# Optimization experiments

Hardware: AMD Instinct MI355X
Metric: run time of the kernel (lower is better)

The kernel has to match this reference:

```python
import jax, jax.numpy as jnp
import numpy as np

H = 2        # num_heads
C = 128      # in_channels
K_ORDER = 4
BETA = 0.5


def _gcn_conv(x, row, col, deg_inv, n):
    # x: [N, H, C]; adj_t = D^{-1} A^T where A[row, col] = 1
    # (adj_t @ x)[c] = deg_inv[c] * sum_{e: col_e == c} x[row_e]
    msg = x[row]  # [E, H, C]
    agg = jax.ops.segment_sum(msg, col, num_segments=n)  # [N, H, C]
    return agg * deg_inv[:, None, None]


def _attn_conv(qs, ks, vs):
    # linear (kernelized) attention, non-block path
    n = qs.shape[0]
    kvs = jnp.einsum('lhm,lhd->hmd', ks, vs)            # [H, C, C]
    qkvs = jnp.einsum('nhm,hmd->nhd', qs, kvs)          # [N, H, C]
    vs_sum = vs.sum(axis=0)                             # [H, C]
    num = qkvs + vs_sum[None, :, :]
    ks_sum = ks.sum(axis=0)                             # [H, C]
    qks_sum = jnp.einsum('nhm,hm->nh', qs, ks_sum)[:, :, None]  # [N, H, 1]
    den = qks_sum + jnp.asarray(n, qs.dtype)
    return num / den


def setup_inputs() -> dict:
    key = jax.random.key(0)
    ks = jax.random.split(key, 8)
    N, E = 100000, 1600000
    x = jax.random.normal(ks[0], (N, C), jnp.float32)
    edge_index = jax.random.randint(ks[1], (2, E), 0, N, jnp.int64)
    s_in = 1.0 / np.sqrt(C)
    s_out = 1.0 / np.sqrt(H * C * (K_ORDER + 1))
    Wq_w = jax.random.normal(ks[2], (C, H * C), jnp.float32) * s_in
    Wq_b = jax.random.normal(ks[3], (H * C,), jnp.float32) * s_in
    Wk_w = jax.random.normal(ks[4], (C, H * C), jnp.float32) * s_in
    Wk_b = jax.random.normal(ks[5], (H * C,), jnp.float32) * s_in
    Wo_w = jax.random.normal(ks[6], (H * C * (K_ORDER + 1), C), jnp.float32) * s_out
    Wo_b = jax.random.normal(ks[7], (C,), jnp.float32) * s_out
    return {"x": x, "edge_index": edge_index, "Wq_w": Wq_w, "Wq_b": Wq_b,
            "Wk_w": Wk_w, "Wk_b": Wk_b, "Wo_w": Wo_w, "Wo_b": Wo_b}


def reference(x, edge_index, Wq_w, Wq_b, Wk_w, Wk_b, Wo_w, Wo_b):
    n = x.shape[0]
    row, col = edge_index[0], edge_index[1]
    # normalized adjacency D^{-1} A^T (pow(-1.0) in the source, not -0.5)
    deg = jax.ops.segment_sum(jnp.ones(row.shape[0], x.dtype), col, num_segments=n)
    deg_inv = jnp.where(deg > 0, 1.0 / deg, 0.0)

    query = (x @ Wq_w + Wq_b).reshape(n, H, C)
    key = (x @ Wk_w + Wk_b).reshape(n, H, C)
    qs = query / jnp.linalg.norm(query, axis=2, keepdims=True)
    ks = key / jnp.linalg.norm(key, axis=2, keepdims=True)

    x0 = jnp.broadcast_to(x[:, None, :], (n, H, C))  # [N, H, C]
    terms = [x0]
    for _ in range(K_ORDER):
        prev = terms[-1]
        gcn_i = _gcn_conv(prev, row, col, deg_inv, n)
        attn_i = _attn_conv(qs, ks, prev)
        terms.append(BETA * gcn_i + attn_i)
    xcat = jnp.concatenate(terms, axis=-1)  # [N, H, C*(K+1)]
    xcat = xcat.reshape(n, H * C * (K_ORDER + 1))
    return (xcat @ Wo_w + Wo_b) / H
```

## Files before the change

### kernel.cpp

```cpp
#include <hip/hip_runtime.h>

#define THREADS 256
#define NB 512
#define SEGCAP 6144
#define CSB 512

typedef __attribute__((ext_vector_type(8))) short short8;
typedef __attribute__((ext_vector_type(4))) float f32x4;

__device__ __forceinline__ float bf2f(unsigned short u) {
    union { unsigned int i; float f; } v;
    v.i = ((unsigned int)u) << 16;
    return v.f;
}
__device__ __forceinline__ unsigned short f2bf(float f) {
    union { float f; unsigned int i; } v;
    v.f = f;
    unsigned int r = (v.i + 0x7FFFu + ((v.i >> 16) & 1u)) >> 16;
    return (unsigned short)r;
}
__device__ __forceinline__ float4 ld4f(const float* p) {
    return *reinterpret_cast<const float4*>(p);
}
__device__ __forceinline__ float4 ld4f(const unsigned short* p) {
// ... 47 lines not shown
    for (int off = 1; off < NB; off <<= 1) {
        int add = (t >= off) ? s[t - off] : 0;
        __syncthreads();
        s[t] += add;
        __syncthreads();
    }
    gbase[t] = s[t] - v;
    gcursor[t] = s[t] - v;
}

__global__ __launch_bounds__(256) void k_part(const int* __restrict__ eb, int E,
                                              const int* __restrict__ mode, int N, int CW, int epb,
                                              int* __restrict__ gcursor, uint2* __restrict__ ebuf) {
    __shared__ int hist[NB];
    __shared__ int base[NB];
    for (int i = threadIdx.x; i < NB; i += 256) hist[i] = 0;
    __syncthreads();
    int m = *mode;
    int e0 = blockIdx.x * epb;
    int e1 = min(e0 + epb, E);
    for (int e = e0 + threadIdx.x; e < e1; e += 256) {
        int c = edge_get(eb, E, m, 1, e);
        if ((unsigned)c < (unsigned)N) atomicAdd(&hist[c / CW], 1);
    }
    __syncthreads();
    for (int i = threadIdx.x; i < NB; i += 256) {
        int h = hist[i];
        base[i] = h ? atomicAdd(&gcursor[i], h) : 0;
        hist[i] = 0;
    }
    __syncthreads();
    for (int e = e0 + threadIdx.x; e < e1; e += 256) {
        int c = edge_get(eb, E, m, 1, e);
        if ((unsigned)c < (unsigned)N) {
            int r = edge_get(eb, E, m, 0, e);
            if ((unsigned)r >= (unsigned)N) r = 0;
            int b = c / CW;
            int li = atomicAdd(&hist[b], 1);
            ebuf[(size_t)base[b] + li] = make_uint2((unsigned)r, (unsigned)c);
        }
    }
}

__global__ __launch_bounds__(256) void k_build(const uint2* __restrict__ ebuf,
                                               const int* __restrict__ gbase,
                                               const int* __restrict__ gcnt, int N, int CW,
                                               int* __restrict__ cnt, int* __restrict__ offs,
                                               float* __restrict__ deg_inv, int* __restrict__ csr) {
    __shared__ int hist[256];
    __shared__ int pfx[256];
    __shared__ int seg[SEGCAP];
    const int b = blockIdx.x;
    const int col0 = b * CW;
    const int ncols = min(CW, N - col0);
    if (ncols <= 0) return;
    const int ebase = gbase[b], ecnt = gcnt[b];
    const int t = threadIdx.x;
    for (int i = t; i < 256; i += 256) hist[i] = 0;
    __syncthreads();
    for (int e = t; e < ecnt; e += 256) {
        uint2 rc = ebuf[(size_t)ebase + e];
        atomicAdd(&hist[rc.y - col0], 1);
    }
    __syncthreads();
    int v = (t < ncols) ? hist[t] : 0;
    pfx[t] = v;
    __syncthreads();
    for (int off = 1; off < 256; off <<= 1) {
        int add = (t >= off) ? pfx[t - off] : 0;
        __syncthreads();
        pfx[t] += add;
        __syncthreads();
    }
    int excl = pfx[t] - v;
    if (t < ncols) {
        cnt[col0 + t] = v;
        offs[col0 + t] = ebase + excl;
        deg_inv[col0 + t] = (v > 0) ? 1.0f / (float)v : 0.0f;
    }
    __syncthreads();
    if (t < 256) hist[t] = (t < ncols) ? excl : 0;
    __syncthreads();
    if (ecnt <= SEGCAP) {
        for (int e = t; e < ecnt; e += 256) {
            uint2 rc = ebuf[(size_t)ebase + e];
            int li = atomicAdd(&hist[rc.y - col0], 1);
            seg[li] = (int)rc.x;
        }
        __syncthreads();
        for (int e = t; e < ecnt; e += 256) csr[(size_t)ebase + e] = seg[e];
    } else {
        for (int e = t; e < ecnt; e += 256) {
            uint2 rc = ebuf[(size_t)ebase + e];
            int li = atomicAdd(&hist[rc.y - col0], 1);
            csr[(size_t)ebase + li] = (int)rc.x;
        }
    }
}

__global__ __launch_bounds__(256) void k_prep_wqk(const float* __restrict__ Wq,
                                                  const float* __restrict__ Wk,
                                                  unsigned short* __restrict__ WqkT) {
    int i = blockIdx.x * 256 + threadIdx.x;
    if (i < 512 * 128) {
        int oc = i >> 7, k = i & 127;
        float v = (oc < 256) ? Wq[k * 256 + oc] : Wk[k * 256 + (oc - 256)];
        WqkT[i] = f2bf(v);
    }
}

__global__ __launch_bounds__(256) void k_prep_wo(const float* __restrict__ Wo,
                                                 unsigned short* __restrict__ WoT) {
    int i = blockIdx.x * 256 + threadIdx.x;
    if (i < 1280 * 128) {
        int r = i >> 7, j = i & 127;
        WoT[(size_t)j * 1280 + r] = f2bf(Wo[i]);
    }
}

__global__ __launch_bounds__(256) void k_prep_wo0(const float* __restrict__ Wo,
                                                  unsigned short* __restrict__ WoT0) {
    int i = blockIdx.x * 256 + threadIdx.x;
    if (i < 16384) {
        int j = i >> 7, c = i & 127;
        WoT0[i] = f2bf(Wo[(size_t)c * 128 + j] + Wo[(size_t)(640 + c) * 128 + j]);
    }
}

__global__ __launch_bounds__(256) void k_proj(const float* __restrict__ x,
                                              const unsigned short* __restrict__ WqkT,
                                              const float* __restrict__ bq,
                                              const float* __restrict__ bk,
                                              unsigned short* __restrict__ qs,
                                              unsigned short* __restrict__ ks, int N) {
    __shared__ unsigned short xs[64 * 128];
    __shared__ unsigned short os[64 * 256];
    const int t = threadIdx.x;
    const int n0 = blockIdx.x * 64;
#pragma unroll
    for (int i = 0; i < 4; i++) {
        int chunk = i * 256 + t;
        int r = chunk >> 4, c0 = (chunk & 15) * 8;
        float4 a0 = make_float4(0.f, 0.f, 0.f, 0.f), a1 = a0;
        if (n0 + r < N) {
            a0 = ld4f(&x[(size_t)(n0 + r) * 128 + c0]);
            a1 = ld4f(&x[(size_t)(n0 + r) * 128 + c0 + 4]);
        }
        short8 v = {(short)f2bf(a0.x), (short)f2bf(a0.y), (short)f2bf(a0.z), (short)f2bf(a0.w),
                    (short)f2bf(a1.x), (short)f2bf(a1.y), (short)f2bf(a1.z), (short)f2bf(a1.w)};
        int byte = r * 256 + ((c0 * 2) ^ ((r & 7) << 4));
        *reinterpret_cast<short8*>(reinterpret_cast<char*>(xs) + byte) = v;
    }
    __syncthreads();
    const int w = t >> 6, l = t & 63, lrow = l & 15, lhi = l >> 4;
    f32x4 acc[4][8];
    const f32x4 fz = {0.f, 0.f, 0.f, 0.f};
#pragma unroll
    for (int mt = 0; mt < 4; mt++)
#pragma unroll
        for (int nt = 0; nt < 8; nt++) acc[mt][nt] = fz;

    for (int kk = 0; kk < 4; kk++) {
        int kb = kk * 32 + lhi * 8;
        short8 af[4];
#pragma unroll
        for (int mt = 0; mt < 4; mt++) {
            int r = mt * 16 + lrow;
            af[mt] = *reinterpret_cast<const short8*>(
                reinterpret_cast<const char*>(xs) + r * 256 + ((kb * 2) ^ ((r & 7) << 4)));
        }
#pragma unroll
        for (int nt = 0; nt < 8; nt++) {
            int oc = w * 128 + nt * 16 + lrow;
            short8 bf = *reinterpret_cast<const short8*>(&WqkT[(size_t)oc * 128 + kb]);
#pragma unroll
            for (int mt = 0; mt < 4; mt++)
                acc[mt][nt] = __builtin_amdgcn_mfma_f32_16x16x32_bf16(af[mt], bf, acc[mt][nt], 0, 0, 0);
        }
    }
#pragma unroll
    for (int nt = 0; nt < 8; nt++) {
        int oc = w * 128 + nt * 16 + lrow;
        float b = (oc < 256) ? bq[oc] : bk[oc - 256];
#pragma unroll
        for (int mt = 0; mt < 4; mt++)
#pragma unroll
            for (int reg = 0; reg < 4; reg++) acc[mt][nt][reg] += b;
    }
    const int hc = (w & 1) * 128;
    float rv[4][4];
#pragma unroll
    for (int mt = 0; mt < 4; mt++) {
        float ss[4] = {0.f, 0.f, 0.f, 0.f};
#pragma unroll
        for (int nt = 0; nt < 8; nt++)
#pragma unroll
            for (int reg = 0; reg < 4; reg++) ss[reg] += acc[mt][nt][reg] * acc[mt][nt][reg];
#pragma unroll
        for (int m_ = 1; m_ < 16; m_ <<= 1)
#pragma unroll
            for (int reg = 0; reg < 4; reg++) ss[reg] += __shfl_xor(ss[reg], m_);
#pragma unroll
        for (int reg = 0; reg < 4; reg++) rv[mt][reg] = rsqrtf(ss[reg]);
    }
    for (int pass = 0; pass < 2; pass++) {
        if ((w >> 1) == pass) {
#pragma unroll
            for (int mt = 0; mt < 4; mt++)
#pragma unroll
                for (int reg = 0; reg < 4; reg++) {
                    int r = mt * 16 + lhi * 4 + reg;
#pragma unroll
                    for (int nt = 0; nt < 8; nt++)
                        os[r * 256 + hc + nt * 16 + lrow] = f2bf(acc[mt][nt][reg] * rv[mt][reg]);
                }
        }
        __syncthreads();
        unsigned short* dstg = pass ? ks : qs;
#pragma unroll
        for (int i = 0; i < 8; i++) {
            int chunk = i * 256 + t;
            int r = chunk >> 5, c = (chunk & 31) * 8;
            int n = n0 + r;
            if (n < N)
                *reinterpret_cast<short8*>(&dstg[(size_t)n * 256 + c]) =
                    *reinterpret_cast<const short8*>(&os[r * 256 + c]);
        }
        __syncthreads();
    }
}

__global__ __launch_bounds__(256) void k_colsum(const unsigned short* __restrict__ ks, int N,
                                                float* __restrict__ part) {
    __shared__ float red[8][256];
    const int t = threadIdx.x;
    const int rl = t >> 5;
    const int c0 = (t & 31) * 8;
    const int stride = (N + CSB - 1) / CSB;
    const int r0 = blockIdx.x * stride;
    const int rend = min(r0 + stride, N);
    float s[8] = {0.f, 0.f, 0.f, 0.f, 0.f, 0.f, 0.f, 0.f};
    int r = r0 + rl;
    for (; r + 24 < rend; r += 32) {
        short8 v0 = *reinterpret_cast<const short8*>(&ks[(size_t)(r + 0) * 256 + c0]);
        short8 v1 = *reinterpret_cast<const short8*>(&ks[(size_t)(r + 8) * 256 + c0]);
        short8 v2 = *reinterpret_cast<const short8*>(&ks[(size_t)(r + 16) * 256 + c0]);
        short8 v3 = *reinterpret_cast<const short8*>(&ks[(size_t)(r + 24) * 256 + c0]);
#pragma unroll
        for (int j = 0; j < 8; j++)
            s[j] += bf2f((unsigned short)v0[j]) + bf2f((unsigned short)v1[j]) +
                    bf2f((unsigned short)v2[j]) + bf2f((unsigned short)v3[j]);
    }
    for (; r < rend; r += 8) {
        short8 v = *reinterpret_cast<const short8*>(&ks[(size_t)r * 256 + c0]);
#pragma unroll
        for (int j = 0; j < 8; j++) s[j] += bf2f((unsigned short)v[j]);
    }
#pragma unroll
    for (int j = 0; j < 8; j++) red[rl][c0 + j] = s[j];
    __syncthreads();
    float tot = 0.f;
#pragma unroll
    for (int g = 0; g < 8; g++) tot += red[g][t];
    part[blockIdx.x * 256 + t] = tot;
}

__global__ __launch_bounds__(256) void k_colsum2(const float* __restrict__ part,
                                                 float* __restrict__ ks_sum) {
    const int t = threadIdx.x;
    float s0 = 0.f, s1 = 0.f, s2 = 0.f, s3 = 0.f;
    for (int b = 0; b < CSB; b += 4) {
        s0 += part[(b + 0) * 256 + t];
        s1 += part[(b + 1) * 256 + t];
        s2 += part[(b + 2) * 256 + t];
        s3 += part[(b + 3) * 256 + t];
    }
    ks_sum[t] = (s0 + s1) + (s2 + s3);
}

__global__ __launch_bounds__(256) void k_den(const unsigned short* __restrict__ qs,
                                             const float* __restrict__ ks_sum,
                                             float* __restrict__ den, int N) {
    int w = threadIdx.x >> 6, lane = threadIdx.x & 63;
    int n = blockIdx.x * 4 + w;
    if (n >= N) return;
    float4 q = ld4f(&qs[(size_t)n * 256 + lane * 4]);
    float4 kv = *reinterpret_cast<const float4*>(&ks_sum[lane * 4]);
    float s = q.x * kv.x + q.y * kv.y + q.z * kv.z + q.w * kv.w;
#pragma unroll
    for (int off = 1; off < 32; off <<= 1) s += __shfl_xor(s, off);
    if ((lane & 31) == 0) den[n * 2 + (lane >> 5)] = s + (float)N;
}

__device__ __forceinline__ short8 frag_ld(const unsigned short* tile, int kb, int col) {
    const char* b = reinterpret_cast<const char*>(tile);
    int cb = (col * 2) ^ (((kb >> 3) & 3) << 5);
    short8 r;
#pragma unroll
    for (int i = 0; i < 8; i++)
        r[i] = (short)*reinterpret_cast<const unsigned short*>(b + (kb + i) * 512 + cb);
    return r;
}

template <typename TV>
__global__ __launch_bounds__(256) void k_kvs2(const unsigned short* __restrict__ ks,
                                              const TV* __restrict__ vs, int vstride, int vmask,
                                              float* __restrict__ partial,
                                              float* __restrict__ pvsum, int rows_per, int N) {
    __shared__ unsigned short kt[32 * 256];
    __shared__ unsigned short vt[32 * 256];
    __shared__ float vred[8][256];
    const int t = threadIdx.x;
    const int w = t >> 6, l = t & 63, lrow = l & 15, lhi = l >> 4;
    const int h = w >> 1, mhalf = w & 1;
    const int r0 = blockIdx.x * rows_per;
    const int rend = min(r0 + rows_per, N);

    const f32x4 fz = {0.f, 0.f, 0.f, 0.f};
    f32x4 acc[4][8];
#pragma unroll
    for (int mt = 0; mt < 4; mt++)
#pragma unroll
        for (int nt = 0; nt < 8; nt++) acc[mt][nt] = fz;
    float vsum8[8] = {0.f, 0.f, 0.f, 0.f, 0.f, 0.f, 0.f, 0.f};

    for (int c0 = r0; c0 < rend; c0 += 32) {
#pragma unroll
        for (int i = 0; i < 4; i++) {
            int chunk = i * 256 + t;
            int n = chunk >> 5, cc = (chunk & 31) * 8;
            short8 v = {0, 0, 0, 0, 0, 0, 0, 0};
            if (c0 + n < rend)
                v = *reinterpret_cast<const short8*>(&ks[(size_t)(c0 + n) * 256 + cc]);
            *reinterpret_cast<short8*>(reinterpret_cast<char*>(kt) + n * 512 +
                                       ((cc * 2) ^ (((n >> 3) & 3) << 5))) = v;
        }
#pragma unroll
        for (int i = 0; i < 4; i++) {
            int chunk = i * 256 + t;
            int n = chunk >> 5, cc = (chunk & 31) * 8;
            float4 a0 = make_float4(0.f, 0.f, 0.f, 0.f), a1 = a0;
            if (c0 + n < rend) {
                a0 = ld4f(&vs[(size_t)(c0 + n) * vstride + (cc & vmask)]);
                a1 = ld4f(&vs[(size_t)(c0 + n) * vstride + ((cc + 4) & vmask)]);
            }
            unsigned short u0 = f2bf(a0.x), u1 = f2bf(a0.y), u2 = f2bf(a0.z), u3 = f2bf(a0.w);
            unsigned short u4 = f2bf(a1.x), u5 = f2bf(a1.y), u6 = f2bf(a1.z), u7 = f2bf(a1.w);
            vsum8[0] += bf2f(u0); vsum8[1] += bf2f(u1); vsum8[2] += bf2f(u2); vsum8[3] += bf2f(u3);
            vsum8[4] += bf2f(u4); vsum8[5] += bf2f(u5); vsum8[6] += bf2f(u6); vsum8[7] += bf2f(u7);
            short8 v = {(short)u0, (short)u1, (short)u2, (short)u3,
                        (short)u4, (short)u5, (short)u6, (short)u7};
            *reinterpret_cast<short8*>(reinterpret_cast<char*>(vt) + n * 512 +
                                       ((cc * 2) ^ (((n >> 3) & 3) << 5))) = v;
        }
        __syncthreads();
        {
            int kb = lhi * 8;
            short8 af[4];
#pragma unroll
            for (int mt = 0; mt < 4; mt++)
                af[mt] = frag_ld(vt, kb, h * 128 + mhalf * 64 + mt * 16 + lrow);
#pragma unroll
            for (int nt = 0; nt < 8; nt++) {
                short8 bf = frag_ld(kt, kb, h * 128 + nt * 16 + lrow);
#pragma unroll
                for (int mt = 0; mt < 4; mt++)
                    acc[mt][nt] =
                        __builtin_amdgcn_mfma_f32_16x16x32_bf16(af[mt], bf, acc[mt][nt], 0, 0, 0);
            }
        }
        __syncthreads();
    }
    float* pb = &partial[((size_t)blockIdx.x * 2 + h) * 16384];
#pragma unroll
    for (int mt = 0; mt < 4; mt++)
#pragma unroll
        for (int reg = 0; reg < 4; reg++) {
            int c_local = mhalf * 64 + mt * 16 + lhi * 4 + reg;
#pragma unroll
            for (int nt = 0; nt < 8; nt++) pb[c_local * 128 + nt * 16 + lrow] = acc[mt][nt][reg];
        }
    {
        int cc = (t & 31) * 8;
#pragma unroll
        for (int j = 0; j < 8; j++) vred[t >> 5][cc + j] = vsum8[j];
        __syncthreads();
        float s = 0.f;
#pragma unroll
        for (int r = 0; r < 8; r++) s += vred[r][t];
        pvsum[blockIdx.x * 256 + t] = s;
    }
}

__global__ __launch_bounds__(256) void k_kvred(const float* __restrict__ partial,
                                               const float* __restrict__ pvsum, int S,
                                               unsigned short* __restrict__ kvsT,
                                               float* __restrict__ vs_sum) {
    if (blockIdx.x == 128) {
        int c = threadIdx.x;
        float s = 0.f;
        for (int i = 0; i < S; i++) s += pvsum[i * 256 + c];
        vs_sum[c] = s;
        return;
    }
    int e = blockIdx.x * 256 + threadIdx.x;
    float s0 = 0.f, s1 = 0.f, s2 = 0.f, s3 = 0.f, s4 = 0.f, s5 = 0.f, s6 = 0.f, s7 = 0.f;
    int i = 0;
    for (; i + 8 <= S; i += 8) {
        s0 += partial[(size_t)(i + 0) * 32768 + e];
        s1 += partial[(size_t)(i + 1) * 32768 + e];
        s2 += partial[(size_t)(i + 2) * 32768 + e];
        s3 += partial[(size_t)(i + 3) * 32768 + e];
        s4 += partial[(size_t)(i + 4) * 32768 + e];
        s5 += partial[(size_t)(i + 5) * 32768 + e];
        s6 += partial[(size_t)(i + 6) * 32768 + e];
        s7 += partial[(size_t)(i + 7) * 32768 + e];
    }
    for (; i < S; i++) s0 += partial[(size_t)i * 32768 + e];
    kvsT[e] = f2bf(((s0 + s1) + (s2 + s3)) + ((s4 + s5) + (s6 + s7)));
}

__global__ __launch_bounds__(256) void k_gather2(const unsigned short* __restrict__ prev,
                                                 const int* __restrict__ csr_src,
                                                 const int* __restrict__ offs,
                                                 const int* __restrict__ cnt,
                                                 const float* __restrict__ deg_inv,
                                                 unsigned short* __restrict__ cur, int N) {
    const int w = threadIdx.x >> 6, l = threadIdx.x & 63;
    int n = blockIdx.x * 4 + w;
    if (n >= N) return;
    const int start = offs[n], d = cnt[n];
    int e = start;
    const int eend = start + d;
    float a0 = 0.f, a1 = 0.f, a2 = 0.f, a3 = 0.f;
    const int co = l * 4;
    for (; e + 16 <= eend; e += 16) {
        int s[16];
#pragma unroll
        for (int i = 0; i < 16; i++) s[i] = csr_src[e + i];
        ushort4 u[16];
#pragma unroll
        for (int i = 0; i < 16; i++)
            u[i] = *reinterpret_cast<const ushort4*>(&prev[(size_t)s[i] * 256 + co]);
#pragma unroll
        for (int i = 0; i < 16; i++) {
            a0 += bf2f(u[i].x); a1 += bf2f(u[i].y); a2 += bf2f(u[i].z); a3 += bf2f(u[i].w);
        }
    }
    for (; e + 8 <= eend; e += 8) {
        int s[8];
#pragma unroll
        for (int i = 0; i < 8; i++) s[i] = csr_src[e + i];
        ushort4 u[8];
#pragma unroll
        for (int i = 0; i < 8; i++)
            u[i] = *reinterpret_cast<const ushort4*>(&prev[(size_t)s[i] * 256 + co]);
#pragma unroll
        for (int i = 0; i < 8; i++) {
            a0 += bf2f(u[i].x); a1 += bf2f(u[i].y); a2 += bf2f(u[i].z); a3 += bf2f(u[i].w);
        }
    }
    for (; e < eend; e++) {
        ushort4 u = *reinterpret_cast<const ushort4*>(&prev[(size_t)csr_src[e] * 256 + co]);
        a0 += bf2f(u.x); a1 += bf2f(u.y); a2 += bf2f(u.z); a3 += bf2f(u.w);
    }
    float sc = 0.5f * deg_inv[n];
    ushort4 o;
    o.x = f2bf(a0 * sc); o.y = f2bf(a1 * sc); o.z = f2bf(a2 * sc); o.w = f2bf(a3 * sc);
    *reinterpret_cast<ushort4*>(&cur[(size_t)n * 256 + co]) = o;
}

__global__ __launch_bounds__(256) void k_gather2f(const float* __restrict__ prev,
                                                  const int* __restrict__ csr_src,
                                                  const int* __restrict__ offs,
                                                  const int* __restrict__ cnt,
                                                  const float* __restrict__ deg_inv,
                                                  unsigned short* __restrict__ cur, int N) {
    const int w = threadIdx.x >> 6, l = threadIdx.x & 63;
    int n = blockIdx.x * 4 + w;
    if (n >= N) return;
    const int start = offs[n], d = cnt[n];
    int e = start;
    const int eend = start + d;
    float a0 = 0.f, a1 = 0.f;
    const int co = l * 2;
    for (; e + 16 <= eend; e += 16) {
        int s[16];
#pragma unroll
        for (int i = 0; i < 16; i++) s[i] = csr_src[e + i];
        float2 u[16];
#pragma unroll
        for (int i = 0; i < 16; i++)
            u[i] = *reinterpret_cast<const float2*>(&prev[(size_t)s[i] * 128 + co]);
#pragma unroll
        for (int i = 0; i < 16; i++) { a0 += u[i].x; a1 += u[i].y; }
    }
    for (; e + 8 <= eend; e += 8) {
        int s[8];
#pragma unroll
        for (int i = 0; i < 8; i++) s[i] = csr_src[e + i];
        float2 u[8];
#pragma unroll
        for (int i = 0; i < 8; i++)
            u[i] = *reinterpret_cast<const float2*>(&prev[(size_t)s[i] * 128 + co]);
#pragma unroll
        for (int i = 0; i < 8; i++) { a0 += u[i].x; a1 += u[i].y; }
    }
    for (; e < eend; e++) {
        float2 u = *reinterpret_cast<const float2*>(&prev[(size_t)csr_src[e] * 128 + co]);
        a0 += u.x; a1 += u.y;
    }
    float sc = 0.5f * deg_inv[n];
    ushort2 o;
    o.x = f2bf(a0 * sc); o.y = f2bf(a1 * sc);
    *reinterpret_cast<ushort2*>(&cur[(size_t)n * 256 + co]) = o;
    *reinterpret_cast<ushort2*>(&cur[(size_t)n * 256 + 128 + co]) = o;
}

__global__ __launch_bounds__(256) void k_att_out(const unsigned short* __restrict__ qs,
                                                 const unsigned short* __restrict__ kvsT,
                                                 const float* __restrict__ vs_sum,
                                                 const float* __restrict__ den,
                                                 unsigned short* __restrict__ cur, int N) {
    __shared__ unsigned short sm[64 * 256];
    const int t = threadIdx.x;
    const int n0 = blockIdx.x * 64;
#pragma unroll
    for (int i = 0; i < 8; i++) {
        int chunk = i * 256 + t;
        int r = chunk >> 5, c0 = (chunk & 31) * 8;
        short8 v = {0, 0, 0, 0, 0, 0, 0, 0};
        if (n0 + r < N) v = *reinterpret_cast<const short8*>(&qs[(size_t)(n0 + r) * 256 + c0]);
        *reinterpret_cast<short8*>(reinterpret_cast<char*>(sm) + r * 512 +
                                   ((c0 * 2) ^ ((r & 7) << 4))) = v;
    }
    short8 cv[8];
#pragma unroll
    for (int i = 0; i < 8; i++) {
        int chunk = i * 256 + t;
        int r = chunk >> 5, c0 = (chunk & 31) * 8;
        short8 v = {0, 0, 0, 0, 0, 0, 0, 0};
        if (n0 + r < N) v = *reinterpret_cast<const short8*>(&cur[(size_t)(n0 + r) * 256 + c0]);
        cv[i] = v;
    }
    __syncthreads();
    const int w = t >> 6, l = t & 63, lrow = l & 15, lhi = l >> 4;
    const int h = w >> 1, jh = w & 1;
    const f32x4 fz = {0.f, 0.f, 0.f, 0.f};
    f32x4 acc[4][4];
#pragma unroll
    for (int mt = 0; mt < 4; mt++)
#pragma unroll
        for (int nt = 0; nt < 4; nt++) acc[mt][nt] = fz;

    for (int kk = 0; kk < 4; kk++) {
        int kb = kk * 32 + lhi * 8;
        short8 af[4];
#pragma unroll
        for (int mt = 0; mt < 4; mt++) {
            int r = mt * 16 + lrow;
            af[mt] = *reinterpret_cast<const short8*>(
                reinterpret_cast<const char*>(sm) + r * 512 +
                (((h * 128 + kb) * 2) ^ ((r & 7) << 4)));
        }
#pragma unroll
        for (int nt = 0; nt < 4; nt++) {
            int c = jh * 64 + nt * 16 + lrow;
            short8 bf = *reinterpret_cast<const short8*>(&kvsT[((size_t)h * 128 + c) * 128 + kb]);
#pragma unroll
            for (int mt = 0; mt < 4; mt++)
                acc[mt][nt] = __builtin_amdgcn_mfma_f32_16x16x32_bf16(af[mt], bf, acc[mt][nt], 0, 0, 0);
        }
    }
    __syncthreads();
#pragma unroll
    for (int mt = 0; mt < 4; mt++) {
#pragma unroll
        for (int reg = 0; reg < 4; reg++) {
            int r = mt * 16 + lhi * 4 + reg;
            int n = n0 + r;
            if (n < N) {
                float idn = 1.0f / den[n * 2 + h];
#pragma unroll
                for (int nt = 0; nt < 4; nt++) {
                    int c = h * 128 + jh * 64 + nt * 16 + lrow;
                    unsigned short* sp = reinterpret_cast<unsigned short*>(
                        reinterpret_cast<char*>(sm) + r * 512 + ((c * 2) ^ ((r & 7) << 4)));
                    *sp = f2bf((acc[mt][nt][reg] + vs_sum[c]) * idn);
                }
            }
        }
    }
    __syncthreads();
#pragma unroll
    for (int i = 0; i < 8; i++) {
        int chunk = i * 256 + t;
        int r = chunk >> 5, c0 = (chunk & 31) * 8;
        int n = n0 + r;
        if (n < N) {
            short8 a = *reinterpret_cast<const short8*>(reinterpret_cast<const char*>(sm) +
                                                        r * 512 + ((c0 * 2) ^ ((r & 7) << 4)));
            short8 o;
#pragma unroll
            for (int j = 0; j < 8; j++)
                o[j] = (short)f2bf(bf2f((unsigned short)cv[i][j]) + bf2f((unsigned short)a[j]));
            *reinterpret_cast<short8*>(&cur[(size_t)n * 256 + c0]) = o;
        }
    }
}

template <int FIRST>
__global__ __launch_bounds__(256) void k_outflush(const float* __restrict__ x,
                                                  const unsigned short* __restrict__ ta,
                                                  const unsigned short* __restrict__ tb,
                                                  const unsigned short* __restrict__ WoT,
                                                  const unsigned short* __restrict__ WoT0,
                                                  const float* __restrict__ Wo_b,
                                                  float* __restrict__ out, int tblkA, int tblkB,
                                                  int N) {
    __shared__ unsigned short sm[64 * 256];
    const int t = threadIdx.x;
    const int n0 = blockIdx.x * 64;
    const int w = t >> 6, l = t & 63, lrow = l & 15, lhi = l >> 4;
    const f32x4 fz = {0.f, 0.f, 0.f, 0.f};
    f32x4 acc2[4][2];
#pragma unroll
    for (int mt = 0; mt < 4; mt++)
#pragma unroll
        for (int nt = 0; nt < 2; nt++) acc2[mt][nt] = fz;

    if (FIRST) {
#pragma unroll
        for (int i = 0; i < 4; i++) {
            int chunk = i * 256 + t;
            int r = chunk >> 4, c0 = (chunk & 15) * 8;
            float4 a0 = make_float4(0.f, 0.f, 0.f, 0.f), a1 = a0;
            if (n0 + r < N) {
                a0 = ld4f(&x[(size_t)(n0 + r) * 128 + c0]);
                a1 = ld4f(&x[(size_t)(n0 + r) * 128 + c0 + 4]);
            }
            short8 v = {(short)f2bf(a0.x), (short)f2bf(a0.y), (short)f2bf(a0.z), (short)f2bf(a0.w),
                        (short)f2bf(a1.x), (short)f2bf(a1.y), (short)f2bf(a1.z), (short)f2bf(a1.w)};
            *reinterpret_cast<short8*>(reinterpret_cast<char*>(sm) + r * 256 +
                                       ((c0 * 2) ^ ((r & 7) << 4))) = v;
        }
        __syncthreads();
        for (int kk = 0; kk < 4; kk++) {
            int kb = kk * 32 + lhi * 8;
            short8 af[4];
#pragma unroll
            for (int mt = 0; mt < 4; mt++) {
                int r = mt * 16 + lrow;
                af[mt] = *reinterpret_cast<const short8*>(
                    reinterpret_cast<const char*>(sm) + r * 256 + ((kb * 2) ^ ((r & 7) << 4)));
            }
#pragma unroll
            for (int nt = 0; nt < 2; nt++) {
                int j = w * 32 + nt * 16 + lrow;
                short8 bf = *reinterpret_cast<const short8*>(&WoT0[(size_t)j * 128 + kb]);
#pragma unroll
                for (int mt = 0; mt < 4; mt++)
                    acc2[mt][nt] =
                        __builtin_amdgcn_mfma_f32_16x16x32_bf16(af[mt], bf, acc2[mt][nt], 0, 0, 0);
            }
        }
        __syncthreads();
    }
#pragma unroll
    for (int b = 0; b < 2; b++) {
        const unsigned short* buf = b ? tb : ta;
        const int tblk = b ? tblkB : tblkA;
#pragma unroll
        for (int i = 0; i < 8; i++) {
            int chunk = i * 256 + t;
            int r = chunk >> 5, c0 = (chunk & 31) * 8;
            short8 v = {0, 0, 0, 0, 0, 0, 0, 0};
            if (n0 + r < N) v = *reinterpret_cast<const short8*>(&buf[(size_t)(n0 + r) * 256 + c0]);
            *reinterpret_cast<short8*>(reinterpret_cast<char*>(sm) + r * 512 +
                                       ((c0 * 2) ^ ((r & 7) << 4))) = v;
        }
        __syncthreads();
        for (int kk = 0; kk < 8; kk++) {
            int kb = kk * 32 + lhi * 8;
            short8 af[4];
#pragma unroll
            for (int mt = 0; mt < 4; mt++) {
                int r = mt * 16 + lrow;
                af[mt] = *reinterpret_cast<const short8*>(
                    reinterpret_cast<const char*>(sm) + r * 512 + ((kb * 2) ^ ((r & 7) << 4)));
            }
            int woff = (kb >> 7) * 640 + tblk * 128 + (kb & 127);
#pragma unroll
            for (int nt = 0; nt < 2; nt++) {
                int j = w * 32 + nt * 16 + lrow;
                short8 bf = *reinterpret_cast<const short8*>(&WoT[(size_t)j * 1280 + woff]);
#pragma unroll
                for (int mt = 0; mt < 4; mt++)
                    acc2[mt][nt] =
                        __builtin_amdgcn_mfma_f32_16x16x32_bf16(af[mt], bf, acc2[mt][nt], 0, 0, 0);
            }
        }
        __syncthreads();
    }
#pragma unroll
    for (int nt = 0; nt < 2; nt++) {
        int j = w * 32 + nt * 16 + lrow;
        float b = FIRST ? Wo_b[j] : 0.f;
#pragma unroll
        for (int mt = 0; mt < 4; mt++)
#pragma unroll
            for (int reg = 0; reg < 4; reg++) {
                int n = n0 + mt * 16 + lhi * 4 + reg;
                if (n < N) {
                    if (FIRST)
                        out[(size_t)n * 128 + j] = 0.5f * (acc2[mt][nt][reg] + b);
                    else
                        out[(size_t)n * 128 + j] += 0.5f * acc2[mt][nt][reg];
                }
            }
    }
}

extern "C" void kernel_launch(void* const* d_in, const int* in_sizes, int n_in,
                              void* d_out, int out_size, void* d_ws, size_t ws_size,
                              hipStream_t stream) {
    const int N = in_sizes[0] / 128;
    const int E = in_sizes[1] / 2;
    const float* x = (const float*)d_in[0];
    const int* eraw = (const int*)d_in[1];
    const float* Wq_w = (const float*)d_in[2];
    const float* Wq_b = (const float*)d_in[3];
    const float* Wk_w = (const float*)d_in[4];
    const float* Wk_b = (const float*)d_in[5];
    const float* Wo_w = (const float*)d_in[6];
    const float* Wo_b = (const float*)d_in[7];
    float* out = (float*)d_out;

    char* p = (char*)d_ws;
    auto alloc = [&](size_t bytes) -> void* {
        void* r = (void*)p;
        p += (bytes + 255) & ~(size_t)255;
        return r;
    };
    unsigned short* qs = (unsigned short*)alloc((size_t)N * 256 * 2);
    unsigned short* ks = (unsigned short*)alloc((size_t)N * 256 * 2);
    unsigned short* bufA = (unsigned short*)alloc((size_t)N * 256 * 2);
    unsigned short* bufB = (unsigned short*)alloc((size_t)N * 256 * 2);
    float* deg_inv = (float*)alloc((size_t)N * 4);
    float* den = (float*)alloc((size_t)N * 2 * 4);
    float* ks_sum = (float*)alloc(256 * 4);
    float* vs_sum = (float*)alloc(256 * 4);
    float* colpart = (float*)alloc((size_t)CSB * 256 * 4);
    unsigned short* WqkT = (unsigned short*)alloc(512 * 128 * 2);
    unsigned short* WoT = (unsigned short*)alloc(1280 * 128 * 2);
    unsigned short* WoT0 = (unsigned short*)alloc(128 * 128 * 2);
    unsigned short* kvsTb = (unsigned short*)alloc(32768 * 2);
    int* cnt = (int*)alloc((size_t)N * 4);
    int* offs = (int*)alloc((size_t)N * 4);
    int* gcnt = (int*)alloc(NB * 4);
    int* gbase = (int*)alloc(NB * 4);
    int* gcursor = (int*)alloc(NB * 4);
    int* mode = (int*)alloc(256);
    int* csr = (int*)alloc((size_t)E * 4);
    uint2* ebuf = (uint2*)alloc((size_t)E * 8);

    size_t used = (size_t)(p - (char*)d_ws);
    size_t rem = (ws_size > used + (1 << 20)) ? ws_size - used - (1 << 20) : 0;
    int S = (int)(rem / (32768 * 4 + 1024));
    if (S > 256) S = 256;
    if (S < 8) S = 8;
    float* partial = (float*)alloc((size_t)S * 32768 * 4);
    float* pvsum = (float*)alloc((size_t)S * 256 * 4);
    const int rows_per = (N + S - 1) / S;

    const int CW = (N + NB - 1) / NB;
    const int EBLK = 256;
    const int epb = (E + EBLK - 1) / EBLK;

    hipMemsetAsync(gcnt, 0, NB * 4, stream);

    k_detect<<<1, 256, 0, stream>>>(eraw, E, mode);
    k_hist<<<EBLK, 256, 0, stream>>>(eraw, E, mode, N, CW, epb, gcnt);
    k_bscan<<<1, NB, 0, stream>>>(gcnt, gbase, gcursor);
    k_part<<<EBLK, 256, 0, stream>>>(eraw, E, mode, N, CW, epb, gcursor, ebuf);
    k_build<<<NB, 256, 0, stream>>>(ebuf, gbase, gcnt, N, CW, cnt, offs, deg_inv, csr);

    k_prep_wqk<<<256, 256, 0, stream>>>(Wq_w, Wk_w, WqkT);
    k_prep_wo<<<640, 256, 0, stream>>>(Wo_w, WoT);
    k_prep_wo0<<<64, 256, 0, stream>>>(Wo_w, WoT0);

    const int nb64 = (N + 63) / 64;
    k_proj<<<nb64, 256, 0, stream>>>(x, WqkT, Wq_b, Wk_b, qs, ks, N);
    k_colsum<<<CSB, 256, 0, stream>>>(ks, N, colpart);
    k_colsum2<<<1, 256, 0, stream>>>(colpart, ks_sum);
    k_den<<<(N + 3) / 4, 256, 0, stream>>>(qs, ks_sum, den, N);

    const int gb4 = (N + 3) / 4;

    k_kvs2<float><<<S, 256, 0, stream>>>(ks, x, 128, 127, partial, pvsum, rows_per, N);
    k_kvred<<<129, 256, 0, stream>>>(partial, pvsum, S, kvsTb, vs_sum);
    k_gather2f<<<gb4, 256, 0, stream>>>(x, csr, offs, cnt, deg_inv, bufA, N);
    k_att_out<<<nb64, 256, 0, stream>>>(qs, kvsTb, vs_sum, den, bufA, N);

    k_kvs2<unsigned short><<<S, 256, 0, stream>>>(ks, bufA, 256, 255, partial, pvsum, rows_per, N);
    k_kvred<<<129, 256, 0, stream>>>(partial, pvsum, S, kvsTb, vs_sum);
    k_gather2<<<gb4, 256, 0, stream>>>(bufA, csr, offs, cnt, deg_inv, bufB, N);
    k_att_out<<<nb64, 256, 0, stream>>>(qs, kvsTb, vs_sum, den, bufB, N);

    k_outflush<1><<<nb64, 256, 0, stream>>>(x, bufA, bufB, WoT, WoT0, Wo_b, out, 1, 2, N);

    k_kvs2<unsigned short><<<S, 256, 0, stream>>>(ks, bufB, 256, 255, partial, pvsum, rows_per, N);
    k_kvred<<<129, 256, 0, stream>>>(partial, pvsum, S, kvsTb, vs_sum);
    k_gather2<<<gb4, 256, 0, stream>>>(bufB, csr, offs, cnt, deg_inv, bufA, N);
    k_att_out<<<nb64, 256, 0, stream>>>(qs, kvsTb, vs_sum, den, bufA, N);

    k_kvs2<unsigned short><<<S, 256, 0, stream>>>(ks, bufA, 256, 255, partial, pvsum, rows_per, N);
    k_kvred<<<129, 256, 0, stream>>>(partial, pvsum, S, kvsTb, vs_sum);
    k_gather2<<<gb4, 256, 0, stream>>>(bufA, csr, offs, cnt, deg_inv, bufB, N);
    k_att_out<<<nb64, 256, 0, stream>>>(qs, kvsTb, vs_sum, den, bufB, N);

    k_outflush<0><<<nb64, 256, 0, stream>>>(x, bufA, bufB, WoT, WoT0, Wo_b, out, 3, 4, N);
}
```

Measured before the change: 1.556 ms.

## Fuse attention output into next kvs pass and final output projection

Drops the separate attention-output kernel. Each term's attention result is now computed inside the next kvs reduction kernel, which writes the finished term and accumulates K^T V in the same pass. The last term's attention is fused into a new output-flush kernel that also applies the Wo projection for terms 3 and 4. The edge buffer is also aliased onto the partial workspace when it fits. This removes several full N x 256 bf16 read and write passes and kernel launches, at the cost of heavier kernels with more syncs and shared-memory reuse.

```diff
diff --git a/kernel.cpp b/kernel.cpp
--- a/kernel.cpp
+++ b/kernel.cpp
@@ -373,11 +373,10 @@
     return r;
 }
 
-template <typename TV>
-__global__ __launch_bounds__(256) void k_kvs2(const unsigned short* __restrict__ ks,
-                                              const TV* __restrict__ vs, int vstride, int vmask,
-                                              float* __restrict__ partial,
-                                              float* __restrict__ pvsum, int rows_per, int N) {
+__global__ __launch_bounds__(256) void k_kvs2x(const unsigned short* __restrict__ ks,
+                                               const float* __restrict__ vs,
+                                               float* __restrict__ partial,
+                                               float* __restrict__ pvsum, int rows_per, int N) {
     __shared__ unsigned short kt[32 * 256];
     __shared__ unsigned short vt[32 * 256];
     __shared__ float vred[8][256];
@@ -412,8 +411,8 @@
             int n = chunk >> 5, cc = (chunk & 31) * 8;
             float4 a0 = make_float4(0.f, 0.f, 0.f, 0.f), a1 = a0;
             if (c0 + n < rend) {
-                a0 = ld4f(&vs[(size_t)(c0 + n) * vstride + (cc & vmask)]);
-                a1 = ld4f(&vs[(size_t)(c0 + n) * vstride + ((cc + 4) & vmask)]);
+                a0 = ld4f(&vs[(size_t)(c0 + n) * 128 + (cc & 127)]);
+                a1 = ld4f(&vs[(size_t)(c0 + n) * 128 + ((cc + 4) & 127)]);
             }
             unsigned short u0 = f2bf(a0.x), u1 = f2bf(a0.y), u2 = f2bf(a0.z), u3 = f2bf(a0.w);
             unsigned short u4 = f2bf(a1.x), u5 = f2bf(a1.y), u6 = f2bf(a1.z), u7 = f2bf(a1.w);
@@ -448,6 +447,159 @@
 #pragma unroll
         for (int reg = 0; reg < 4; reg++) {
             int c_local = mhalf * 64 + mt * 16 + lhi * 4 + reg;
+#pragma unroll
+            for (int nt = 0; nt < 8; nt++) pb[c_local * 128 + nt * 16 + lrow] = acc[mt][nt][reg];
+        }
+    {
+        int cc = (t & 31) * 8;
+#pragma unroll
+        for (int j = 0; j < 8; j++) vred[t >> 5][cc + j] = vsum8[j];
+        __syncthreads();
+        float s = 0.f;
+#pragma unroll
+        for (int r = 0; r < 8; r++) s += vred[r][t];
+        pvsum[blockIdx.x * 256 + t] = s;
+    }
+}
+
+__global__ __launch_bounds__(256) void k_kvsterm(const unsigned short* __restrict__ ks,
+                                                 const unsigned short* __restrict__ qs,
+                                                 const unsigned short* __restrict__ gbuf,
+                                                 const unsigned short* __restrict__ kvsTp,
+                                                 const float* __restrict__ vs_sum_p,
+                                                 const float* __restrict__ den,
+                                                 unsigned short* __restrict__ cur,
+                                                 float* __restrict__ partial,
+                                                 float* __restrict__ pvsum, int rows_per, int N) {
+    __shared__ unsigned short kt[32 * 256];
+    __shared__ unsigned short vt[32 * 256];
+    __shared__ float vred[8][256];
+    const int t = threadIdx.x;
+    const int w = t >> 6, l = t & 63, lrow = l & 15, lhi = l >> 4;
+    const int h = w >> 1, jh = w & 1;
+    const int r0 = blockIdx.x * rows_per;
+    const int rend = min(r0 + rows_per, N);
+
+    const f32x4 fz = {0.f, 0.f, 0.f, 0.f};
+    f32x4 acc[4][8];
+#pragma unroll
+    for (int mt = 0; mt < 4; mt++)
+#pragma unroll
+        for (int nt = 0; nt < 8; nt++) acc[mt][nt] = fz;
+    float vsum8[8] = {0.f, 0.f, 0.f, 0.f, 0.f, 0.f, 0.f, 0.f};
+
+    for (int c0 = r0; c0 < rend; c0 += 32) {
+#pragma unroll
+        for (int i = 0; i < 4; i++) {
+            int chunk = i * 256 + t;
+            int r = chunk >> 5, cc = (chunk & 31) * 8;
+            int n = c0 + r;
+            short8 g = {0, 0, 0, 0, 0, 0, 0, 0}, q = g;
+            if (n < rend) {
+                g = *reinterpret_cast<const short8*>(&gbuf[(size_t)n * 256 + cc]);
+                q = *reinterpret_cast<const short8*>(&qs[(size_t)n * 256 + cc]);
+            }
+            int swz = (cc * 2) ^ ((r & 7) << 4);
+            *reinterpret_cast<short8*>(reinterpret_cast<char*>(kt) + r * 512 + swz) = g;
+            *reinterpret_cast<short8*>(reinterpret_cast<char*>(vt) + r * 512 + swz) = q;
+        }
+        __syncthreads();
+        f32x4 acc2[2][4];
+#pragma unroll
+        for (int mt = 0; mt < 2; mt++)
+#pragma unroll
+            for (int nt = 0; nt < 4; nt++) acc2[mt][nt] = fz;
+        for (int kk = 0; kk < 4; kk++) {
+            int kb = kk * 32 + lhi * 8;
+            short8 af[2];
+#pragma unroll
+            for (int mt = 0; mt < 2; mt++) {
+                int r = mt * 16 + lrow;
+                af[mt] = *reinterpret_cast<const short8*>(
+                    reinterpret_cast<const char*>(vt) + r * 512 +
+                    (((h * 128 + kb) * 2) ^ ((r & 7) << 4)));
+            }
+#pragma unroll
+            for (int nt = 0; nt < 4; nt++) {
+                int c = jh * 64 + nt * 16 + lrow;
+                short8 bf =
+                    *reinterpret_cast<const short8*>(&kvsTp[((size_t)h * 128 + c) * 128 + kb]);
+#pragma unroll
+                for (int mt = 0; mt < 2; mt++)
+                    acc2[mt][nt] =
+                        __builtin_amdgcn_mfma_f32_16x16x32_bf16(af[mt], bf, acc2[mt][nt], 0, 0, 0);
+            }
+        }
+        __syncthreads();
+#pragma unroll
+        for (int mt = 0; mt < 2; mt++) {
+#pragma unroll
+            for (int reg = 0; reg < 4; reg++) {
+                int r = mt * 16 + lhi * 4 + reg;
+                int n = c0 + r;
+                if (n < rend) {
+                    float idn = 1.0f / den[n * 2 + h];
+#pragma unroll
+                    for (int nt = 0; nt < 4; nt++) {
+                        int c = h * 128 + jh * 64 + nt * 16 + lrow;
+                        float g = bf2f(*reinterpret_cast<const unsigned short*>(
+                            reinterpret_cast<const char*>(kt) + r * 512 +
+                            ((c * 2) ^ ((r & 7) << 4))));
+                        float v = g + (acc2[mt][nt][reg] + vs_sum_p[c]) * idn;
+                        *reinterpret_cast<unsigned short*>(reinterpret_cast<char*>(vt) + r * 512 +
+                                                           ((c * 2) ^ (((r >> 3) & 3) << 5))) =
+                            f2bf(v);
+                    }
+                } else {
+#pragma unroll
+                    for (int nt = 0; nt < 4; nt++) {
+                        int c = h * 128 + jh * 64 + nt * 16 + lrow;
+                        *reinterpret_cast<unsigned short*>(reinterpret_cast<char*>(vt) + r * 512 +
+                                                           ((c * 2) ^ (((r >> 3) & 3) << 5))) = 0;
+                    }
+                }
+            }
+        }
+        __syncthreads();
+#pragma unroll
+        for (int i = 0; i < 4; i++) {
+            int chunk = i * 256 + t;
+            int r = chunk >> 5, cc = (chunk & 31) * 8;
+            int n = c0 + r;
+            short8 v = *reinterpret_cast<const short8*>(
+                reinterpret_cast<const char*>(vt) + r * 512 + ((cc * 2) ^ (((r >> 3) & 3) << 5)));
+#pragma unroll
+            for (int j = 0; j < 8; j++) vsum8[j] += bf2f((unsigned short)v[j]);
+            if (n < rend) *reinterpret_cast<short8*>(&cur[(size_t)n * 256 + cc]) = v;
+            short8 kv = {0, 0, 0, 0, 0, 0, 0, 0};
+            if (n < rend) kv = *reinterpret_cast<const short8*>(&ks[(size_t)n * 256 + cc]);
+            *reinterpret_cast<short8*>(reinterpret_cast<char*>(kt) + r * 512 +
+                                       ((cc * 2) ^ (((r >> 3) & 3) << 5))) = kv;
+        }
+        __syncthreads();
+        {
+            int kb = lhi * 8;
+            short8 af[4];
+#pragma unroll
+            for (int mt = 0; mt < 4; mt++)
+                af[mt] = frag_ld(vt, kb, h * 128 + jh * 64 + mt * 16 + lrow);
+#pragma unroll
+            for (int nt = 0; nt < 8; nt++) {
+                short8 bf = frag_ld(kt, kb, h * 128 + nt * 16 + lrow);
+#pragma unroll
+                for (int mt = 0; mt < 4; mt++)
+                    acc[mt][nt] =
+                        __builtin_amdgcn_mfma_f32_16x16x32_bf16(af[mt], bf, acc[mt][nt], 0, 0, 0);
+            }
+        }
+        __syncthreads();
+    }
+    float* pb = &partial[((size_t)blockIdx.x * 2 + h) * 16384];
+#pragma unroll
+    for (int mt = 0; mt < 4; mt++)
+#pragma unroll
+        for (int reg = 0; reg < 4; reg++) {
+            int c_local = jh * 64 + mt * 16 + lhi * 4 + reg;
 #pragma unroll
             for (int nt = 0; nt < 8; nt++) pb[c_local * 128 + nt * 16 + lrow] = acc[mt][nt][reg];
         }
@@ -588,98 +740,6 @@
     *reinterpret_cast<ushort2*>(&cur[(size_t)n * 256 + 128 + co]) = o;
 }
 
-__global__ __launch_bounds__(256) void k_att_out(const unsigned short* __restrict__ qs,
-                                                 const unsigned short* __restrict__ kvsT,
-                                                 const float* __restrict__ vs_sum,
-                                                 const float* __restrict__ den,
-                                                 unsigned short* __restrict__ cur, int N) {
-    __shared__ unsigned short sm[64 * 256];
-    const int t = threadIdx.x;
-    const int n0 = blockIdx.x * 64;
-#pragma unroll
-    for (int i = 0; i < 8; i++) {
-        int chunk = i * 256 + t;
-        int r = chunk >> 5, c0 = (chunk & 31) * 8;
-        short8 v = {0, 0, 0, 0, 0, 0, 0, 0};
-        if (n0 + r < N) v = *reinterpret_cast<const short8*>(&qs[(size_t)(n0 + r) * 256 + c0]);
-        *reinterpret_cast<short8*>(reinterpret_cast<char*>(sm) + r * 512 +
-                                   ((c0 * 2) ^ ((r & 7) << 4))) = v;
-    }
-    short8 cv[8];
-#pragma unroll
-    for (int i = 0; i < 8; i++) {
-        int chunk = i * 256 + t;
-        int r = chunk >> 5, c0 = (chunk & 31) * 8;
-        short8 v = {0, 0, 0, 0, 0, 0, 0, 0};
-        if (n0 + r < N) v = *reinterpret_cast<const short8*>(&cur[(size_t)(n0 + r) * 256 + c0]);
-        cv[i] = v;
-    }
-    __syncthreads();
-    const int w = t >> 6, l = t & 63, lrow = l & 15, lhi = l >> 4;
-    const int h = w >> 1, jh = w & 1;
-    const f32x4 fz = {0.f, 0.f, 0.f, 0.f};
-    f32x4 acc[4][4];
-#pragma unroll
-    for (int mt = 0; mt < 4; mt++)
-#pragma unroll
-        for (int nt = 0; nt < 4; nt++) acc[mt][nt] = fz;
-
-    for (int kk = 0; kk < 4; kk++) {
-        int kb = kk * 32 + lhi * 8;
-        short8 af[4];
-#pragma unroll
-        for (int mt = 0; mt < 4; mt++) {
-            int r = mt * 16 + lrow;
-            af[mt] = *reinterpret_cast<const short8*>(
-                reinterpret_cast<const char*>(sm) + r * 512 +
-                (((h * 128 + kb) * 2) ^ ((r & 7) << 4)));
-        }
-#pragma unroll
-        for (int nt = 0; nt < 4; nt++) {
-            int c = jh * 64 + nt * 16 + lrow;
-            short8 bf = *reinterpret_cast<const short8*>(&kvsT[((size_t)h * 128 + c) * 128 + kb]);
-#pragma unroll
-            for (int mt = 0; mt < 4; mt++)
-                acc[mt][nt] = __builtin_amdgcn_mfma_f32_16x16x32_bf16(af[mt], bf, acc[mt][nt], 0, 0, 0);
-        }
-    }
-    __syncthreads();
-#pragma unroll
-    for (int mt = 0; mt < 4; mt++) {
-#pragma unroll
-        for (int reg = 0; reg < 4; reg++) {
-            int r = mt * 16 + lhi * 4 + reg;
-            int n = n0 + r;
-            if (n < N) {
-                float idn = 1.0f / den[n * 2 + h];
-#pragma unroll
-                for (int nt = 0; nt < 4; nt++) {
-                    int c = h * 128 + jh * 64 + nt * 16 + lrow;
-                    unsigned short* sp = reinterpret_cast<unsigned short*>(
-                        reinterpret_cast<char*>(sm) + r * 512 + ((c * 2) ^ ((r & 7) << 4)));
-                    *sp = f2bf((acc[mt][nt][reg] + vs_sum[c]) * idn);
-                }
-            }
-        }
-    }
-    __syncthreads();
-#pragma unroll
-    for (int i = 0; i < 8; i++) {
-        int chunk = i * 256 + t;
-        int r = chunk >> 5, c0 = (chunk & 31) * 8;
-        int n = n0 + r;
-        if (n < N) {
-            short8 a = *reinterpret_cast<const short8*>(reinterpret_cast<const char*>(sm) +
-                                                        r * 512 + ((c0 * 2) ^ ((r & 7) << 4)));
-            short8 o;
-#pragma unroll
-            for (int j = 0; j < 8; j++)
-                o[j] = (short)f2bf(bf2f((unsigned short)cv[i][j]) + bf2f((unsigned short)a[j]));
-            *reinterpret_cast<short8*>(&cur[(size_t)n * 256 + c0]) = o;
-        }
-    }
-}
-
 template <int FIRST>
 __global__ __launch_bounds__(256) void k_outflush(const float* __restrict__ x,
                                                   const unsigned short* __restrict__ ta,
@@ -792,6 +852,164 @@
     }
 }
 
+__global__ __launch_bounds__(256) void k_outflush2(const unsigned short* __restrict__ qs,
+                                                   const unsigned short* __restrict__ gbuf,
+                                                   const unsigned short* __restrict__ kvsT,
+                                                   const float* __restrict__ vs_sum,
+                                                   const float* __restrict__ den,
+                                                   const unsigned short* __restrict__ t3,
+                                                   const unsigned short* __restrict__ WoT,
+                                                   float* __restrict__ out, int N) {
+    __shared__ unsigned short sm[64 * 256];
+    const int t = threadIdx.x;
+    const int n0 = blockIdx.x * 64;
+    const int w = t >> 6, l = t & 63, lrow = l & 15, lhi = l >> 4;
+    const f32x4 fz = {0.f, 0.f, 0.f, 0.f};
+
+    short8 cv[8];
+#pragma unroll
+    for (int i = 0; i < 8; i++) {
+        int chunk = i * 256 + t;
+        int r = chunk >> 5, c0 = (chunk & 31) * 8;
+        short8 v = {0, 0, 0, 0, 0, 0, 0, 0};
+        if (n0 + r < N) v = *reinterpret_cast<const short8*>(&gbuf[(size_t)(n0 + r) * 256 + c0]);
+        cv[i] = v;
+    }
+#pragma unroll
+    for (int i = 0; i < 8; i++) {
+        int chunk = i * 256 + t;
+        int r = chunk >> 5, c0 = (chunk & 31) * 8;
+        short8 v = {0, 0, 0, 0, 0, 0, 0, 0};
+        if (n0 + r < N) v = *reinterpret_cast<const short8*>(&qs[(size_t)(n0 + r) * 256 + c0]);
+        *reinterpret_cast<short8*>(reinterpret_cast<char*>(sm) + r * 512 +
+                                   ((c0 * 2) ^ ((r & 7) << 4))) = v;
+    }
+    __syncthreads();
+    const int h = w >> 1, jh = w & 1;
+    f32x4 acc[4][4];
+#pragma unroll
+    for (int mt = 0; mt < 4; mt++)
+#pragma unroll
+        for (int nt = 0; nt < 4; nt++) acc[mt][nt] = fz;
+    for (int kk = 0; kk < 4; kk++) {
+        int kb = kk * 32 + lhi * 8;
+        short8 af[4];
+#pragma unroll
+        for (int mt = 0; mt < 4; mt++) {
+            int r = mt * 16 + lrow;
+            af[mt] = *reinterpret_cast<const short8*>(
+                reinterpret_cast<const char*>(sm) + r * 512 +
+                (((h * 128 + kb) * 2) ^ ((r & 7) << 4)));
+        }
+#pragma unroll
+        for (int nt = 0; nt < 4; nt++) {
+            int c = jh * 64 + nt * 16 + lrow;
+            short8 bf = *reinterpret_cast<const short8*>(&kvsT[((size_t)h * 128 + c) * 128 + kb]);
+#pragma unroll
+            for (int mt = 0; mt < 4; mt++)
+                acc[mt][nt] = __builtin_amdgcn_mfma_f32_16x16x32_bf16(af[mt], bf, acc[mt][nt], 0, 0, 0);
+        }
+    }
+    __syncthreads();
+#pragma unroll
+    for (int mt = 0; mt < 4; mt++) {
+#pragma unroll
+        for (int reg = 0; reg < 4; reg++) {
+            int r = mt * 16 + lhi * 4 + reg;
+            int n = n0 + r;
+            if (n < N) {
+                float idn = 1.0f / den[n * 2 + h];
+#pragma unroll
+                for (int nt = 0; nt < 4; nt++) {
+                    int c = h * 128 + jh * 64 + nt * 16 + lrow;
+                    *reinterpret_cast<unsigned short*>(reinterpret_cast<char*>(sm) + r * 512 +
+                                                       ((c * 2) ^ ((r & 7) << 4))) =
+                        f2bf((acc[mt][nt][reg] + vs_sum[c]) * idn);
+                }
+            }
+        }
+    }
+    __syncthreads();
+#pragma unroll
+    for (int i = 0; i < 8; i++) {
+        int chunk = i * 256 + t;
+        int r = chunk >> 5, c0 = (chunk & 31) * 8;
+        char* loc = reinterpret_cast<char*>(sm) + r * 512 + ((c0 * 2) ^ ((r & 7) << 4));
+        short8 a = *reinterpret_cast<const short8*>(loc);
+        short8 o;
+#pragma unroll
+        for (int j = 0; j < 8; j++)
+            o[j] = (short)f2bf(bf2f((unsigned short)cv[i][j]) + bf2f((unsigned short)a[j]));
+        *reinterpret_cast<short8*>(loc) = o;
+    }
+    __syncthreads();
+    f32x4 acc2[4][2];
+#pragma unroll
+    for (int mt = 0; mt < 4; mt++)
+#pragma unroll
+        for (int nt = 0; nt < 2; nt++) acc2[mt][nt] = fz;
+    for (int kk = 0; kk < 8; kk++) {
+        int kb = kk * 32 + lhi * 8;
+        short8 af[4];
+#pragma unroll
+        for (int mt = 0; mt < 4; mt++) {
+            int r = mt * 16 + lrow;
+            af[mt] = *reinterpret_cast<const short8*>(
+                reinterpret_cast<const char*>(sm) + r * 512 + ((kb * 2) ^ ((r & 7) << 4)));
+        }
+        int woff = (kb >> 7) * 640 + 4 * 128 + (kb & 127);
+#pragma unroll
+        for (int nt = 0; nt < 2; nt++) {
+            int j = w * 32 + nt * 16 + lrow;
+            short8 bf = *reinterpret_cast<const short8*>(&WoT[(size_t)j * 1280 + woff]);
+#pragma unroll
+            for (int mt = 0; mt < 4; mt++)
+                acc2[mt][nt] = __builtin_amdgcn_mfma_f32_16x16x32_bf16(af[mt], bf, acc2[mt][nt], 0, 0, 0);
+        }
+    }
+    __syncthreads();
+#pragma unroll
+    for (int i = 0; i < 8; i++) {
+        int chunk = i * 256 + t;
+        int r = chunk >> 5, c0 = (chunk & 31) * 8;
+        short8 v = {0, 0, 0, 0, 0, 0, 0, 0};
+        if (n0 + r < N) v = *reinterpret_cast<const short8*>(&t3[(size_t)(n0 + r) * 256 + c0]);
+        *reinterpret_cast<short8*>(reinterpret_cast<char*>(sm) + r * 512 +
+                                   ((c0 * 2) ^ ((r & 7) << 4))) = v;
+    }
+    __syncthreads();
+    for (int kk = 0; kk < 8; kk++) {
+        int kb = kk * 32 + lhi * 8;
+        short8 af[4];
+#pragma unroll
+        for (int mt = 0; mt < 4; mt++) {
+            int r = mt * 16 + lrow;
+            af[mt] = *reinterpret_cast<const short8*>(
+                reinterpret_cast<const char*>(sm) + r * 512 + ((kb * 2) ^ ((r & 7) << 4)));
+        }
+        int woff = (kb >> 7) * 640 + 3 * 128 + (kb & 127);
+#pragma unroll
+        for (int nt = 0; nt < 2; nt++) {
+            int j = w * 32 + nt * 16 + lrow;
+            short8 bf = *reinterpret_cast<const short8*>(&WoT[(size_t)j * 1280 + woff]);
+#pragma unroll
+            for (int mt = 0; mt < 4; mt++)
+                acc2[mt][nt] = __builtin_amdgcn_mfma_f32_16x16x32_bf16(af[mt], bf, acc2[mt][nt], 0, 0, 0);
+        }
+    }
+#pragma unroll
+    for (int nt = 0; nt < 2; nt++) {
+        int j = w * 32 + nt * 16 + lrow;
+#pragma unroll
+        for (int mt = 0; mt < 4; mt++)
+#pragma unroll
+            for (int reg = 0; reg < 4; reg++) {
+                int n = n0 + mt * 16 + lhi * 4 + reg;
+                if (n < N) out[(size_t)n * 128 + j] += 0.5f * acc2[mt][nt][reg];
+            }
+    }
+}
+
 extern "C" void kernel_launch(void* const* d_in, const int* in_sizes, int n_in,
                               void* d_out, int out_size, void* d_ws, size_t ws_size,
                               hipStream_t stream) {
@@ -815,8 +1033,8 @@
     };
     unsigned short* qs = (unsigned short*)alloc((size_t)N * 256 * 2);
     unsigned short* ks = (unsigned short*)alloc((size_t)N * 256 * 2);
-    unsigned short* bufA = (unsigned short*)alloc((size_t)N * 256 * 2);
-    unsigned short* bufB = (unsigned short*)alloc((size_t)N * 256 * 2);
+    unsigned short* B1 = (unsigned short*)alloc((size_t)N * 256 * 2);
+    unsigned short* B2 = (unsigned short*)alloc((size_t)N * 256 * 2);
     float* deg_inv = (float*)alloc((size_t)N * 4);
     float* den = (float*)alloc((size_t)N * 2 * 4);
     float* ks_sum = (float*)alloc(256 * 4);
@@ -833,7 +1051,6 @@
     int* gcursor = (int*)alloc(NB * 4);
     int* mode = (int*)alloc(256);
     int* csr = (int*)alloc((size_t)E * 4);
-    uint2* ebuf = (uint2*)alloc((size_t)E * 8);
 
     size_t used = (size_t)(p - (char*)d_ws);
     size_t rem = (ws_size > used + (1 << 20)) ? ws_size - used - (1 << 20) : 0;
@@ -842,6 +1059,11 @@
     if (S < 8) S = 8;
     float* partial = (float*)alloc((size_t)S * 32768 * 4);
     float* pvsum = (float*)alloc((size_t)S * 256 * 4);
+    uint2* ebuf;
+    if ((size_t)S * 32768 * 4 >= (size_t)E * 8)
+        ebuf = (uint2*)partial;
+    else
+        ebuf = (uint2*)alloc((size_t)E * 8);
     const int rows_per = (N + S - 1) / S;
 
     const int CW = (N + NB - 1) / NB;
@@ -868,27 +1090,25 @@
 
     const int gb4 = (N + 3) / 4;
 
-    k_kvs2<float><<<S, 256, 0, stream>>>(ks, x, 128, 127, partial, pvsum, rows_per, N);
+    k_kvs2x<<<S, 256, 0, stream>>>(ks, x, partial, pvsum, rows_per, N);
     k_kvred<<<129, 256, 0, stream>>>(partial, pvsum, S, kvsTb, vs_sum);
-    k_gather2f<<<gb4, 256, 0, stream>>>(x, csr, offs, cnt, deg_inv, bufA, N);
-    k_att_out<<<nb64, 256, 0, stream>>>(qs, kvsTb, vs_sum, den, bufA, N);
-
-    k_kvs2<unsigned short><<<S, 256, 0, stream>>>(ks, bufA, 256, 255, partial, pvsum, rows_per, N);
+    k_gather2f<<<gb4, 256, 0, stream>>>(x, csr, offs, cnt, deg_inv, B1, N);
+
+    k_kvsterm<<<S, 256, 0, stream>>>(ks, qs, B1, kvsTb, vs_sum, den, B1, partial, pvsum,
+                                     rows_per, N);
     k_kvred<<<129, 256, 0, stream>>>(partial, pvsum, S, kvsTb, vs_sum);
-    k_gather2<<<gb4, 256, 0, stream>>>(bufA, csr, offs, cnt, deg_inv, bufB, N);
-    k_att_out<<<nb64, 256, 0, stream>>>(qs, kvsTb, vs_sum, den, bufB, N);
-
-    k_outflush<1><<<nb64, 256, 0, stream>>>(x, bufA, bufB, WoT, WoT0, Wo_b, out, 1, 2, N);
-
-    k_kvs2<unsigned short><<<S, 256, 0, stream>>>(ks, bufB, 256, 255, partial, pvsum, rows_per, N);
+    k_gather2<<<gb4, 256, 0, stream>>>(B1, csr, offs, cnt, deg_inv, B2, N);
+
+    k_kvsterm<<<S, 256, 0, stream>>>(ks, qs, B2, kvsTb, vs_sum, den, B2, partial, pvsum,
+                                     rows_per, N);
     k_kvred<<<129, 256, 0, stream>>>(partial, pvsum, S, kvsTb, vs_sum);
-    k_gather2<<<gb4, 256, 0, stream>>>(bufB, csr, offs, cnt, deg_inv, bufA, N);
-    k_att_out<<<nb64, 256, 0, stream>>>(qs, kvsTb, vs_sum, den, bufA, N);
-
-    k_kvs2<unsigned short><<<S, 256, 0, stream>>>(ks, bufA, 256, 255, partial, pvsum, rows_per, N);
+    k_outflush<1><<<nb64, 256, 0, stream>>>(x, B1, B2, WoT, WoT0, Wo_b, out, 1, 2, N);
+    k_gather2<<<gb4, 256, 0, stream>>>(B2, csr, offs, cnt, deg_inv, B1, N);
+
+    k_kvsterm<<<S, 256, 0, stream>>>(ks, qs, B1, kvsTb, vs_sum, den, B1, partial, pvsum,
+                                     rows_per, N);
     k_kvred<<<129, 256, 0, stream>>>(partial, pvsum, S, kvsTb, vs_sum);
-    k_gather2<<<gb4, 256, 0, stream>>>(bufA, csr, offs, cnt, deg_inv, bufB, N);
-    k_att_out<<<nb64, 256, 0, stream>>>(qs, kvsTb, vs_sum, den, bufB, N);
-
-    k_outflush<0><<<nb64, 256, 0, stream>>>(x, bufA, bufB, WoT, WoT0, Wo_b, out, 3, 4, N);
-}
+    k_gather2<<<gb4, 256, 0, stream>>>(B1, csr, offs, cnt, deg_inv, B2, N);
+
+    k_outflush2<<<nb64, 256, 0, stream>>>(qs, B2, kvsTb, vs_sum, den, B1, WoT, out, N);
+}
```

Measured after the change: 1.560 ms. No clear change (+0.3%).
